# Kernel tuning notes

Measured on AMD Instinct MI355X. Metric: run time of the kernel, lower is better.

## Reference

```python
import jax, jax.numpy as jnp
import numpy as np

T, B, IN = 512, 256, 64
INNER = 20


def _lin_params(key, fan_in, fan_out):
    k1, k2 = jax.random.split(key)
    bound = 1.0 / np.sqrt(fan_in)
    w = jax.random.uniform(k1, (fan_out, fan_in), jnp.float32, -bound, bound)
    b = jax.random.uniform(k2, (fan_out,), jnp.float32, -bound, bound)
    return w, b


def _rnn_params(key, in_sz, hid):
    k1, k2, k3, k4 = jax.random.split(key, 4)
    bound = 1.0 / np.sqrt(hid)
    wih = jax.random.uniform(k1, (hid, in_sz), jnp.float32, -bound, bound)
    whh = jax.random.uniform(k2, (hid, hid), jnp.float32, -bound, bound)
    bih = jax.random.uniform(k3, (hid,), jnp.float32, -bound, bound)
    bhh = jax.random.uniform(k4, (hid,), jnp.float32, -bound, bound)
    return wih, whh, bih, bhh


def setup_inputs() -> dict:
    key = jax.random.key(0)
    ks = jax.random.split(key, 9)
    x = jax.random.normal(ks[0], (T, B, IN), jnp.float32)
    e_w1, e_b1 = _lin_params(ks[1], IN, 128)
    e_w2, e_b2 = _lin_params(ks[2], 128, 64)
    e_w3, e_b3 = _lin_params(ks[3], 64, 32)
    r1_wih, r1_whh, r1_bih, r1_bhh = _rnn_params(ks[4], 32, INNER)
    r2_wih, r2_whh, r2_bih, r2_bhh = _rnn_params(ks[5], INNER, 32)
    d_w1, d_b1 = _lin_params(ks[6], 32, 64)
    d_w2, d_b2 = _lin_params(ks[7], 64, 128)
    d_w3, d_b3 = _lin_params(ks[8], 128, IN)
    return dict(x=x,
                e_w1=e_w1, e_b1=e_b1, e_w2=e_w2, e_b2=e_b2, e_w3=e_w3, e_b3=e_b3,
                r1_wih=r1_wih, r1_whh=r1_whh, r1_bih=r1_bih, r1_bhh=r1_bhh,
                r2_wih=r2_wih, r2_whh=r2_whh, r2_bih=r2_bih, r2_bhh=r2_bhh,
                d_w1=d_w1, d_b1=d_b1, d_w2=d_w2, d_b2=d_b2, d_w3=d_w3, d_b3=d_b3)


def _rnn(x, wih, whh, bih, bhh):
    # x: (T, B, F); vanilla tanh RNN, h0 = 0. Returns all hidden states (T, B, H).
    # Precompute input projection for all timesteps in one GEMM.
    xp = jnp.einsum('tbf,hf->tbh', x, wih) + bih + bhh
    h0 = jnp.zeros((x.shape[1], whh.shape[0]), x.dtype)

    def step(h, xt):
        h = jnp.tanh(xt + h @ whh.T)
        return h, h

    _, out = jax.lax.scan(step, h0, xp)
    return out


def reference(x,
              e_w1, e_b1, e_w2, e_b2, e_w3, e_b3,
              r1_wih, r1_whh, r1_bih, r1_bhh,
              r2_wih, r2_whh, r2_bih, r2_bhh,
              d_w1, d_b1, d_w2, d_b2, d_w3, d_b3):
    relu = jax.nn.relu
    # encoder MLP
    h = relu(x @ e_w1.T + e_b1)
    h = relu(h @ e_w2.T + e_b2)
    h = relu(h @ e_w3.T + e_b3)
    # encoder RNN -> code (T, B, INNER)
    code = _rnn(h, r1_wih, r1_whh, r1_bih, r1_bhh)
    # decoder RNN then ReLU
    d = relu(_rnn(code, r2_wih, r2_whh, r2_bih, r2_bhh))
    d = relu(d @ d_w1.T + d_b1)
    d = relu(d @ d_w2.T + d_b2)
    return d @ d_w3.T + d_b3
```

## Files before the change

kernel.cpp:

```cpp
#include <hip/hip_runtime.h>

typedef _Float16 half8 __attribute__((ext_vector_type(8)));
typedef _Float16 half2_t __attribute__((ext_vector_type(2)));
typedef float f32x4 __attribute__((ext_vector_type(4)));

#define MFMA16(a, b, c) __builtin_amdgcn_mfma_f32_16x16x32_f16((a), (b), (c), 0, 0, 0)

__device__ __forceinline__ float exp2_fast(float x) {
#if __has_builtin(__builtin_amdgcn_exp2f)
    return __builtin_amdgcn_exp2f(x);
#else
    return exp2f(x);
#endif
}

__device__ __forceinline__ float tanh_fast(float x) {
    x = fminf(x, 22.f);
    float e = exp2_fast(2.885390082f * x);
    return (e - 1.f) * __builtin_amdgcn_rcpf(e + 1.f);
}

__device__ __forceinline__ float dot2f(unsigned a, unsigned b, float c) {
#if __has_builtin(__builtin_amdgcn_fdot2)
    return __builtin_amdgcn_fdot2(__builtin_bit_cast(half2_t, a),
                                  __builtin_bit_cast(half2_t, b), c, false);
#else
    float d;
    asm("v_dot2_f32_f16 %0, %1, %2, %3" : "=v"(d) : "v"(a), "v"(b), "v"(c));
    return d;
#endif
}


__global__ __launch_bounds__(256) void prep_kernel(
    const float* __restrict__ e_w1, const float* __restrict__ e_w3,
    const float* __restrict__ r1_wih, const float* __restrict__ e_w2,
    const float* __restrict__ d_w1, const float* __restrict__ d_w2,
    const float* __restrict__ d_w3,
    const float* __restrict__ r1_whh, const float* __restrict__ r2_wih,
    const float* __restrict__ r2_whh,
    const float* __restrict__ r2_bih, const float* __restrict__ r2_bhh,
    _Float16* __restrict__ enc_img, _Float16* __restrict__ w2img,
    _Float16* __restrict__ dec_img, _Float16* __restrict__ dw3img,
    unsigned* __restrict__ rnn_img)
{
    int i = blockIdx.x * 256 + threadIdx.x;
    if (i < 8192) {
        int r = i >> 6, c = i & 63;
        enc_img[r * 72 + c] = (_Float16)e_w1[i];
    } else if (i < 10240) {
        int j = i - 8192; int r = j >> 6, c = j & 63;
        enc_img[9216 + r * 72 + c] = (_Float16)e_w3[j];
    } else if (i < 10880) {
        int j = i - 10240; int r = j >> 5, c = j & 31;
        enc_img[11520 + r * 40 + c] = (_Float16)r1_wih[j];
    } else if (i < 19072) {
        int j = i - 10880;
        w2img[j] = (_Float16)e_w2[j];
    } else if (i < 21120) {
        int j = i - 19072; int r = j >> 5, c = j & 31;
        dec_img[r * 40 + c] = (_Float16)d_w1[j];
    } else if (i < 29312) {
        int j = i - 21120; int r = j >> 6, c = j & 63;
        dec_img[2560 + r * 72 + c] = (_Float16)d_w2[j];
    } else if (i < 37504) {
        int j = i - 29312;
        dw3img[j] = (_Float16)d_w3[j];
    } else if (i < 39552) {
        int j = i - 37504;
        int row = j >> 5, c = j & 31;
        unsigned val = 0;
        if (c == 26) {
            float b = (row < 32) ? (r2_bih[row] + r2_bhh[row]) : 0.f;
            val = __builtin_bit_cast(unsigned, b);
        } else {
            float v0 = 0.f, v1 = 0.f;
            if (row < 32) {
                if (c < 10)      { v0 = r2_wih[row * 20 + 2*c]; v1 = r2_wih[row * 20 + 2*c + 1]; }
                else if (c < 26) { int k = c - 10;
                                   v0 = r2_whh[row * 32 + 2*k]; v1 = r2_whh[row * 32 + 2*k + 1]; }
            } else if (row < 52) {
                int uu = row - 32;
                if (c < 10)      { v0 = r1_whh[uu * 20 + 2*c]; v1 = r1_whh[uu * 20 + 2*c + 1]; }
            }
            unsigned lo = (unsigned)__builtin_bit_cast(unsigned short, (_Float16)v0);
            unsigned hi = (unsigned)__builtin_bit_cast(unsigned short, (_Float16)v1);
            val = lo | (hi << 16);
        }
        rnn_img[j] = val;
    }
}

__global__ __launch_bounds__(256) void enc_kernel(
    const float* __restrict__ x,
    const float* __restrict__ eb1, const float* __restrict__ eb2,
    const float* __restrict__ eb3,
    const float* __restrict__ r1bih, const float* __restrict__ r1bhh,
    const _Float16* __restrict__ enc_img, const _Float16* __restrict__ w2img,
    float* __restrict__ xp1)
{
    __shared__ _Float16 a1buf[64 * 136];
    __shared__ _Float16 a2buf[64 * 72];
    __shared__ _Float16 a3buf[64 * 40];

    const int tid  = threadIdx.x;
    const int lane = tid & 63;
    const int wv   = tid >> 6;
    const int l15  = lane & 15;
    const int kg   = lane >> 4;
    const int rowA  = blockIdx.x * 64 + wv * 16 + l15;
    const int rowDl = wv * 16 + kg * 4;
    const int rowDg = blockIdx.x * 64 + rowDl;

    half8 a0, a1f;
    {
        const float* xr = x + (size_t)rowA * 64 + kg * 8;
        f32x4 p0 = *(const f32x4*)(xr);
        f32x4 p1 = *(const f32x4*)(xr + 4);
        f32x4 p2 = *(const f32x4*)(xr + 32);
        f32x4 p3 = *(const f32x4*)(xr + 36);
        #pragma unroll
        for (int j = 0; j < 4; ++j) {
            a0[j]    = (_Float16)p0[j];
            a0[j+4]  = (_Float16)p1[j];
            a1f[j]   = (_Float16)p2[j];
            a1f[j+4] = (_Float16)p3[j];
        }
    }
    f32x4 acc1[8] = {};
    #pragma unroll
    for (int ct = 0; ct < 8; ++ct) {
        const _Float16* wp = enc_img + (ct * 16 + l15) * 72 + kg * 8;
        half8 b0 = *(const half8*)(wp);
        half8 b1 = *(const half8*)(wp + 32);
        acc1[ct] = MFMA16(a0, b0, acc1[ct]);
        acc1[ct] = MFMA16(a1f, b1, acc1[ct]);
    }
    #pragma unroll
    for (int ct = 0; ct < 8; ++ct) {
        int col = ct * 16 + l15;
        float b = eb1[col];
        #pragma unroll
        for (int r = 0; r < 4; ++r) {
            float v = fmaxf(acc1[ct][r] + b, 0.f);
            a1buf[(rowDl + r) * 136 + col] = (_Float16)v;
        }
    }

    half8 af[4];
    #pragma unroll
    for (int kt = 0; kt < 4; ++kt)
        af[kt] = *(const half8*)(a1buf + (wv * 16 + l15) * 136 + kt * 32 + kg * 8);
    f32x4 acc2[4] = {};
    #pragma unroll
    for (int ct = 0; ct < 4; ++ct) {
        const _Float16* wp = w2img + (ct * 16 + l15) * 128 + kg * 8;
        #pragma unroll
        for (int kt = 0; kt < 4; ++kt) {
            half8 b = *(const half8*)(wp + kt * 32);
            acc2[ct] = MFMA16(af[kt], b, acc2[ct]);
        }
    }
    #pragma unroll
    for (int ct = 0; ct < 4; ++ct) {
        int col = ct * 16 + l15;
        float b = eb2[col];
        #pragma unroll
        for (int r = 0; r < 4; ++r) {
            float v = fmaxf(acc2[ct][r] + b, 0.f);
            a2buf[(rowDl + r) * 72 + col] = (_Float16)v;
        }
    }

    half8 c0 = *(const half8*)(a2buf + (wv * 16 + l15) * 72 + kg * 8);
    half8 c1 = *(const half8*)(a2buf + (wv * 16 + l15) * 72 + 32 + kg * 8);
    f32x4 acc3[2] = {};
    #pragma unroll
    for (int ct = 0; ct < 2; ++ct) {
        const _Float16* wp = enc_img + 9216 + (ct * 16 + l15) * 72 + kg * 8;
        half8 b0 = *(const half8*)(wp);
        half8 b1 = *(const half8*)(wp + 32);
        acc3[ct] = MFMA16(c0, b0, acc3[ct]);
        acc3[ct] = MFMA16(c1, b1, acc3[ct]);
    }
    #pragma unroll
    for (int ct = 0; ct < 2; ++ct) {
        int col = ct * 16 + l15;
        float b = eb3[col];
        #pragma unroll
        for (int r = 0; r < 4; ++r) {
            float v = fmaxf(acc3[ct][r] + b, 0.f);
            a3buf[(rowDl + r) * 40 + col] = (_Float16)v;
        }
    }

    half8 d0 = *(const half8*)(a3buf + (wv * 16 + l15) * 40 + kg * 8);
    f32x4 acc4[2] = {};
    #pragma unroll
    for (int ct = 0; ct < 2; ++ct) {
        const _Float16* wp = enc_img + 11520 + (ct * 16 + l15) * 40 + kg * 8;
        half8 b0 = *(const half8*)(wp);
        acc4[ct] = MFMA16(d0, b0, acc4[ct]);
    }
    #pragma unroll
    for (int ct = 0; ct < 2; ++ct) {
        int col = ct * 16 + l15;
        if (col < 20) {
            float bs = r1bih[col] + r1bhh[col];
            #pragma unroll
            for (int r = 0; r < 4; ++r)
                xp1[(size_t)(rowDg + r) * 20 + col] = acc4[ct][r] + bs;
        }
    }
}

__global__ __launch_bounds__(64) void rnn_kernel(
    const float* __restrict__ xp1,
    const unsigned* __restrict__ rnn_img,
    _Float16* __restrict__ dbuf)
{
    const int lane  = threadIdx.x & 63;
    const int batch = blockIdx.x;

    unsigned w[26];
    float base_b;
    {
        const unsigned* wr = rnn_img + lane * 32;
        #pragma unroll
        for (int i = 0; i < 6; ++i) {
            uint4 q = *(const uint4*)(wr + i * 4);
            w[i*4+0] = q.x; w[i*4+1] = q.y; w[i*4+2] = q.z; w[i*4+3] = q.w;
        }
        uint4 q = *(const uint4*)(wr + 24);
        w[24] = q.x; w[25] = q.y;
        base_b = __builtin_bit_cast(float, q.z);
    }

    const bool isB = lane < 32;
    int ua = lane - 32;
    if (ua < 0 || ua > 19) ua = 0;
    const float* xcol = xp1 + (size_t)batch * 20 + ua;

    const size_t DUMP_ELEMS = 4198400;
    _Float16* dst = isB ? (dbuf + (size_t)batch * 32 + lane)
                        : (dbuf + DUMP_ELEMS + (size_t)batch * 64 + lane);
    const size_t dstride = isB ? 8192 : 0;

    const unsigned sel = (lane & 1) ? 0x01000504u : 0x05040100u;
    unsigned hs[26];

    {
        float x0 = xcol[0];
        float h0 = isB ? 0.f : tanh_fast(x0);
        _Float16 h16 = (_Float16)h0;
        unsigned own  = (unsigned)__builtin_bit_cast(unsigned short, h16);
        unsigned dppv = (unsigned)__builtin_amdgcn_update_dpp(0, (int)own, 0xB1, 0xF, 0xF, false);
        unsigned pk   = __builtin_amdgcn_perm(dppv, own, sel);
        #pragma unroll
        for (int i = 0; i < 10; ++i)
            hs[i]    = (unsigned)__builtin_amdgcn_ds_bpermute((32 + 2*i) * 4, (int)pk);
        #pragma unroll
        for (int i = 0; i < 16; ++i)
            hs[10+i] = (unsigned)__builtin_amdgcn_ds_bpermute((2*i) * 4, (int)pk);
    }

    float xr[8];
    #pragma unroll
    for (int j = 0; j < 8; ++j)
        xr[j] = xcol[(size_t)(1 + j) * 5120];

    #pragma unroll 1
    for (int t0 = 0; t0 < 512; t0 += 8) {
        #pragma unroll
        for (int j = 0; j < 8; ++j) {
            const int t = t0 + j;
            float a0 = isB ? base_b : xr[j];
            float a1 = 0.f, a2 = 0.f, a3 = 0.f, a4 = 0.f, a5 = 0.f, a6 = 0.f, a7 = 0.f;
            a0 = dot2f(w[0],  hs[0],  a0);
            a1 = dot2f(w[1],  hs[1],  a1);
            a2 = dot2f(w[2],  hs[2],  a2);
            a3 = dot2f(w[3],  hs[3],  a3);
            a4 = dot2f(w[4],  hs[4],  a4);
            a5 = dot2f(w[5],  hs[5],  a5);
            a6 = dot2f(w[6],  hs[6],  a6);
            a7 = dot2f(w[7],  hs[7],  a7);
            a0 = dot2f(w[8],  hs[8],  a0);
            a1 = dot2f(w[9],  hs[9],  a1);
            a2 = dot2f(w[10], hs[10], a2);
            a3 = dot2f(w[11], hs[11], a3);
            a4 = dot2f(w[12], hs[12], a4);
            a5 = dot2f(w[13], hs[13], a5);
            a6 = dot2f(w[14], hs[14], a6);
            a7 = dot2f(w[15], hs[15], a7);
            a0 = dot2f(w[16], hs[16], a0);
            a1 = dot2f(w[17], hs[17], a1);
            a2 = dot2f(w[18], hs[18], a2);
            a3 = dot2f(w[19], hs[19], a3);
            a4 = dot2f(w[20], hs[20], a4);
            a5 = dot2f(w[21], hs[21], a5);
            a6 = dot2f(w[22], hs[22], a6);
            a7 = dot2f(w[23], hs[23], a7);
            a0 = dot2f(w[24], hs[24], a0);
            a1 = dot2f(w[25], hs[25], a1);
            float r = ((a0 + a1) + (a2 + a3)) + ((a4 + a5) + (a6 + a7));
            float h = tanh_fast(r);
            _Float16 h16 = (_Float16)h;

            _Float16 z = (_Float16)0.f;
            *dst = (h16 > z) ? h16 : z;
            dst += dstride;

            unsigned own  = (unsigned)__builtin_bit_cast(unsigned short, h16);
            unsigned dppv = (unsigned)__builtin_amdgcn_update_dpp(0, (int)own, 0xB1, 0xF, 0xF, false);
            unsigned pk   = __builtin_amdgcn_perm(dppv, own, sel);
            #pragma unroll
            for (int i = 0; i < 10; ++i)
                hs[i]    = (unsigned)__builtin_amdgcn_ds_bpermute((32 + 2*i) * 4, (int)pk);
            #pragma unroll
            for (int i = 0; i < 16; ++i)
                hs[10+i] = (unsigned)__builtin_amdgcn_ds_bpermute((2*i) * 4, (int)pk);

            xr[j] = xcol[(size_t)(t + 9) * 5120];
        }
    }
}

__global__ __launch_bounds__(256) void dec_kernel(
    const _Float16* __restrict__ dbuf,
    const float* __restrict__ db1, const float* __restrict__ db2,
    const float* __restrict__ db3,
    const _Float16* __restrict__ dec_img, const _Float16* __restrict__ dw3img,
    float* __restrict__ out)
{
    __shared__ _Float16 a1buf[64 * 72];
    __shared__ _Float16 a2buf[64 * 136];

    const int tid  = threadIdx.x;
    const int lane = tid & 63;
    const int wv   = tid >> 6;
    const int l15  = lane & 15;
    const int kg   = lane >> 4;
    const int rowA  = blockIdx.x * 64 + wv * 16 + l15;
    const int rowDl = wv * 16 + kg * 4;
    const int rowDg = blockIdx.x * 64 + rowDl;

    half8 a0 = *(const half8*)(dbuf + (size_t)rowA * 32 + kg * 8);
    f32x4 acc1[4] = {};
    #pragma unroll
    for (int ct = 0; ct < 4; ++ct) {
        half8 b = *(const half8*)(dec_img + (ct * 16 + l15) * 40 + kg * 8);
        acc1[ct] = MFMA16(a0, b, acc1[ct]);
    }
    #pragma unroll
    for (int ct = 0; ct < 4; ++ct) {
        int col = ct * 16 + l15;
        float b = db1[col];
        #pragma unroll
        for (int r = 0; r < 4; ++r) {
            float v = fmaxf(acc1[ct][r] + b, 0.f);
            a1buf[(rowDl + r) * 72 + col] = (_Float16)v;
        }
    }

    half8 af0 = *(const half8*)(a1buf + (wv * 16 + l15) * 72 + kg * 8);
    half8 af1 = *(const half8*)(a1buf + (wv * 16 + l15) * 72 + 32 + kg * 8);
    f32x4 acc2[8] = {};
    #pragma unroll
    for (int ct = 0; ct < 8; ++ct) {
        const _Float16* wp = dec_img + 2560 + (ct * 16 + l15) * 72 + kg * 8;
        half8 b0 = *(const half8*)(wp);
        half8 b1 = *(const half8*)(wp + 32);
        acc2[ct] = MFMA16(af0, b0, acc2[ct]);
        acc2[ct] = MFMA16(af1, b1, acc2[ct]);
    }
    #pragma unroll
    for (int ct = 0; ct < 8; ++ct) {
        int col = ct * 16 + l15;
        float b = db2[col];
        #pragma unroll
        for (int r = 0; r < 4; ++r) {
            float v = fmaxf(acc2[ct][r] + b, 0.f);
            a2buf[(rowDl + r) * 136 + col] = (_Float16)v;
        }
    }

    half8 cf[4];
    #pragma unroll
    for (int kt = 0; kt < 4; ++kt)
        cf[kt] = *(const half8*)(a2buf + (wv * 16 + l15) * 136 + kt * 32 + kg * 8);
    f32x4 acc3[4] = {};
    #pragma unroll
    for (int ct = 0; ct < 4; ++ct) {
        const _Float16* wp = dw3img + (ct * 16 + l15) * 128 + kg * 8;
        #pragma unroll
        for (int kt = 0; kt < 4; ++kt) {
            half8 b = *(const half8*)(wp + kt * 32);
            acc3[ct] = MFMA16(cf[kt], b, acc3[ct]);
        }
    }
    #pragma unroll
    for (int ct = 0; ct < 4; ++ct) {
        int col = ct * 16 + l15;
        float b = db3[col];
        #pragma unroll
        for (int r = 0; r < 4; ++r)
            out[(size_t)(rowDg + r) * 64 + col] = acc3[ct][r] + b;
    }
}

extern "C" void kernel_launch(void* const* d_in, const int* in_sizes, int n_in,
                              void* d_out, int out_size, void* d_ws, size_t ws_size,
                              hipStream_t stream) {
    const float* x      = (const float*)d_in[0];
    const float* e_w1   = (const float*)d_in[1];
    const float* e_b1   = (const float*)d_in[2];
    const float* e_w2   = (const float*)d_in[3];
    const float* e_b2   = (const float*)d_in[4];
    const float* e_w3   = (const float*)d_in[5];
    const float* e_b3   = (const float*)d_in[6];
    const float* r1_wih = (const float*)d_in[7];
    const float* r1_whh = (const float*)d_in[8];
    const float* r1_bih = (const float*)d_in[9];
    const float* r1_bhh = (const float*)d_in[10];
    const float* r2_wih = (const float*)d_in[11];
    const float* r2_whh = (const float*)d_in[12];
    const float* r2_bih = (const float*)d_in[13];
    const float* r2_bhh = (const float*)d_in[14];
    const float* d_w1   = (const float*)d_in[15];
    const float* d_b1   = (const float*)d_in[16];
    const float* d_w2   = (const float*)d_in[17];
    const float* d_b2   = (const float*)d_in[18];
    const float* d_w3   = (const float*)d_in[19];
    const float* d_b3   = (const float*)d_in[20];

    char* ws = (char*)d_ws;
    _Float16* enc_img = (_Float16*)(ws + 0);
    _Float16* w2img   = (_Float16*)(ws + 25600);
    _Float16* dec_img = (_Float16*)(ws + 41984);
    _Float16* dw3img  = (_Float16*)(ws + 65536);
    float*    xp1     = (float*)(ws + 81920);
    _Float16* dbuf    = (_Float16*)(ws + 10567680);
    unsigned* rnn_img = (unsigned*)(ws + 18956288);

    prep_kernel<<<155, 256, 0, stream>>>(e_w1, e_w3, r1_wih, e_w2, d_w1, d_w2, d_w3,
                                         r1_whh, r2_wih, r2_whh, r2_bih, r2_bhh,
                                         enc_img, w2img, dec_img, dw3img, rnn_img);
    enc_kernel<<<2048, 256, 0, stream>>>(x, e_b1, e_b2, e_b3, r1_bih, r1_bhh,
                                         enc_img, w2img, xp1);
    rnn_kernel<<<256, 64, 0, stream>>>(xp1, rnn_img, dbuf);
    dec_kernel<<<2048, 256, 0, stream>>>(dbuf, d_b1, d_b2, d_b3, dec_img, dw3img,
                                         (float*)d_out);
}
```

Before: 152.3 us.

## Permute weight columns for packed fp16 epilogue stores and store RNN input projection in fp16

Weight images are column-permuted in prep so each lane's MFMA output columns become contiguous. The bias+ReLU epilogues can then write packed fp16 vectors to LDS (uint4/uint2) instead of scalar halves. Biases are folded into accumulator initialisation. The RNN input projection xp1 is now stored as fp16 with a padded, permuted 32-wide layout rather than fp32, which halves its traffic at some precision cost, and the RNN kernel's dbuf write order and read indexing are adjusted to match.

After: 155.2 us. About the same (+1.9%).

```diff
diff --git a/kernel.cpp b/kernel.cpp
--- a/kernel.cpp
+++ b/kernel.cpp
@@ -2,6 +2,7 @@
 
 typedef _Float16 half8 __attribute__((ext_vector_type(8)));
 typedef _Float16 half2_t __attribute__((ext_vector_type(2)));
+typedef __fp16 fp16x2 __attribute__((ext_vector_type(2)));
 typedef float f32x4 __attribute__((ext_vector_type(4)));
 
 #define MFMA16(a, b, c) __builtin_amdgcn_mfma_f32_16x16x32_f16((a), (b), (c), 0, 0, 0)
@@ -29,6 +30,15 @@
     asm("v_dot2_f32_f16 %0, %1, %2, %3" : "=v"(d) : "v"(a), "v"(b), "v"(c));
     return d;
 #endif
+}
+
+__device__ __forceinline__ unsigned pk_relu(float a, float b) {
+    fp16x2 h = __builtin_amdgcn_cvt_pkrtz(fmaxf(a, 0.f), fmaxf(b, 0.f));
+    return __builtin_bit_cast(unsigned, h);
+}
+__device__ __forceinline__ unsigned pk2(float a, float b) {
+    fp16x2 h = __builtin_amdgcn_cvt_pkrtz(a, b);
+    return __builtin_bit_cast(unsigned, h);
 }
 
 
@@ -50,24 +60,25 @@
         enc_img[r * 72 + c] = (_Float16)e_w1[i];
     } else if (i < 10240) {
         int j = i - 8192; int r = j >> 6, c = j & 63;
-        enc_img[9216 + r * 72 + c] = (_Float16)e_w3[j];
-    } else if (i < 10880) {
-        int j = i - 10240; int r = j >> 5, c = j & 31;
-        enc_img[11520 + r * 40 + c] = (_Float16)r1_wih[j];
-    } else if (i < 19072) {
-        int j = i - 10880;
-        w2img[j] = (_Float16)e_w2[j];
-    } else if (i < 21120) {
-        int j = i - 19072; int r = j >> 5, c = j & 31;
-        dec_img[r * 40 + c] = (_Float16)d_w1[j];
-    } else if (i < 29312) {
-        int j = i - 21120; int r = j >> 6, c = j & 63;
-        dec_img[2560 + r * 72 + c] = (_Float16)d_w2[j];
-    } else if (i < 37504) {
-        int j = i - 29312;
-        dw3img[j] = (_Float16)d_w3[j];
-    } else if (i < 39552) {
-        int j = i - 37504;
+        enc_img[9216 + r * 72 + ((c & 15) * 4 + (c >> 4))] = (_Float16)e_w3[j];
+    } else if (i < 11264) {
+        int j = i - 10240; int r = j >> 5, k = j & 31;
+        float v = (r < 20) ? r1_wih[r * 32 + k] : 0.f;
+        enc_img[11520 + r * 32 + ((k & 15) * 2 + (k >> 4))] = (_Float16)v;
+    } else if (i < 19456) {
+        int j = i - 11264; int r = j >> 7, c = j & 127;
+        w2img[r * 128 + ((c & 15) * 8 + (c >> 4))] = (_Float16)e_w2[j];
+    } else if (i < 21504) {
+        int j = i - 19456; int r = j >> 5, k = j & 31;
+        dec_img[r * 32 + ((k & 15) * 2 + (k >> 4))] = (_Float16)d_w1[j];
+    } else if (i < 29696) {
+        int j = i - 21504; int r = j >> 6, c = j & 63;
+        dec_img[2048 + r * 72 + ((c & 15) * 4 + (c >> 4))] = (_Float16)d_w2[j];
+    } else if (i < 37888) {
+        int j = i - 29696; int r = j >> 7, c = j & 127;
+        dw3img[r * 128 + ((c & 15) * 8 + (c >> 4))] = (_Float16)d_w3[j];
+    } else if (i < 39936) {
+        int j = i - 37888;
         int row = j >> 5, c = j & 31;
         unsigned val = 0;
         if (c == 26) {
@@ -97,7 +108,7 @@
     const float* __restrict__ eb3,
     const float* __restrict__ r1bih, const float* __restrict__ r1bhh,
     const _Float16* __restrict__ enc_img, const _Float16* __restrict__ w2img,
-    float* __restrict__ xp1)
+    unsigned* __restrict__ xp1u)
 {
     __shared__ _Float16 a1buf[64 * 136];
     __shared__ _Float16 a2buf[64 * 72];
@@ -127,7 +138,12 @@
             a1f[j+4] = (_Float16)p3[j];
         }
     }
-    f32x4 acc1[8] = {};
+    f32x4 acc1[8];
+    #pragma unroll
+    for (int ct = 0; ct < 8; ++ct) {
+        float b = eb1[ct * 16 + l15];
+        acc1[ct] = (f32x4){b, b, b, b};
+    }
     #pragma unroll
     for (int ct = 0; ct < 8; ++ct) {
         const _Float16* wp = enc_img + (ct * 16 + l15) * 72 + kg * 8;
@@ -137,21 +153,25 @@
         acc1[ct] = MFMA16(a1f, b1, acc1[ct]);
     }
     #pragma unroll
-    for (int ct = 0; ct < 8; ++ct) {
-        int col = ct * 16 + l15;
-        float b = eb1[col];
-        #pragma unroll
-        for (int r = 0; r < 4; ++r) {
-            float v = fmaxf(acc1[ct][r] + b, 0.f);
-            a1buf[(rowDl + r) * 136 + col] = (_Float16)v;
-        }
+    for (int r = 0; r < 4; ++r) {
+        uint4 v;
+        v.x = pk_relu(acc1[0][r], acc1[1][r]);
+        v.y = pk_relu(acc1[2][r], acc1[3][r]);
+        v.z = pk_relu(acc1[4][r], acc1[5][r]);
+        v.w = pk_relu(acc1[6][r], acc1[7][r]);
+        *(uint4*)(a1buf + (rowDl + r) * 136 + l15 * 8) = v;
     }
 
     half8 af[4];
     #pragma unroll
     for (int kt = 0; kt < 4; ++kt)
         af[kt] = *(const half8*)(a1buf + (wv * 16 + l15) * 136 + kt * 32 + kg * 8);
-    f32x4 acc2[4] = {};
+    f32x4 acc2[4];
+    #pragma unroll
+    for (int ct = 0; ct < 4; ++ct) {
+        float b = eb2[ct * 16 + l15];
+        acc2[ct] = (f32x4){b, b, b, b};
+    }
     #pragma unroll
     for (int ct = 0; ct < 4; ++ct) {
         const _Float16* wp = w2img + (ct * 16 + l15) * 128 + kg * 8;
@@ -162,19 +182,21 @@
         }
     }
     #pragma unroll
-    for (int ct = 0; ct < 4; ++ct) {
-        int col = ct * 16 + l15;
-        float b = eb2[col];
-        #pragma unroll
-        for (int r = 0; r < 4; ++r) {
-            float v = fmaxf(acc2[ct][r] + b, 0.f);
-            a2buf[(rowDl + r) * 72 + col] = (_Float16)v;
-        }
+    for (int r = 0; r < 4; ++r) {
+        uint2 v;
+        v.x = pk_relu(acc2[0][r], acc2[1][r]);
+        v.y = pk_relu(acc2[2][r], acc2[3][r]);
+        *(uint2*)(a2buf + (rowDl + r) * 72 + l15 * 4) = v;
     }
 
     half8 c0 = *(const half8*)(a2buf + (wv * 16 + l15) * 72 + kg * 8);
     half8 c1 = *(const half8*)(a2buf + (wv * 16 + l15) * 72 + 32 + kg * 8);
-    f32x4 acc3[2] = {};
+    f32x4 acc3[2];
+    #pragma unroll
+    for (int ct = 0; ct < 2; ++ct) {
+        float b = eb3[ct * 16 + l15];
+        acc3[ct] = (f32x4){b, b, b, b};
+    }
     #pragma unroll
     for (int ct = 0; ct < 2; ++ct) {
         const _Float16* wp = enc_img + 9216 + (ct * 16 + l15) * 72 + kg * 8;
@@ -184,38 +206,32 @@
         acc3[ct] = MFMA16(c1, b1, acc3[ct]);
     }
     #pragma unroll
+    for (int r = 0; r < 4; ++r)
+        *(unsigned*)(a3buf + (rowDl + r) * 40 + l15 * 2) =
+            pk_relu(acc3[0][r], acc3[1][r]);
+
+    half8 d0 = *(const half8*)(a3buf + (wv * 16 + l15) * 40 + kg * 8);
+    f32x4 acc4[2];
+    {
+        int c1i = 16 + l15; if (c1i > 19) c1i = 19;
+        float b0v = r1bih[l15] + r1bhh[l15];
+        float b1v = r1bih[c1i] + r1bhh[c1i];
+        acc4[0] = (f32x4){b0v, b0v, b0v, b0v};
+        acc4[1] = (f32x4){b1v, b1v, b1v, b1v};
+    }
+    #pragma unroll
     for (int ct = 0; ct < 2; ++ct) {
-        int col = ct * 16 + l15;
-        float b = eb3[col];
-        #pragma unroll
-        for (int r = 0; r < 4; ++r) {
-            float v = fmaxf(acc3[ct][r] + b, 0.f);
-            a3buf[(rowDl + r) * 40 + col] = (_Float16)v;
-        }
-    }
-
-    half8 d0 = *(const half8*)(a3buf + (wv * 16 + l15) * 40 + kg * 8);
-    f32x4 acc4[2] = {};
-    #pragma unroll
-    for (int ct = 0; ct < 2; ++ct) {
-        const _Float16* wp = enc_img + 11520 + (ct * 16 + l15) * 40 + kg * 8;
+        const _Float16* wp = enc_img + 11520 + (ct * 16 + l15) * 32 + kg * 8;
         half8 b0 = *(const half8*)(wp);
         acc4[ct] = MFMA16(d0, b0, acc4[ct]);
     }
     #pragma unroll
-    for (int ct = 0; ct < 2; ++ct) {
-        int col = ct * 16 + l15;
-        if (col < 20) {
-            float bs = r1bih[col] + r1bhh[col];
-            #pragma unroll
-            for (int r = 0; r < 4; ++r)
-                xp1[(size_t)(rowDg + r) * 20 + col] = acc4[ct][r] + bs;
-        }
-    }
+    for (int r = 0; r < 4; ++r)
+        xp1u[(size_t)(rowDg + r) * 16 + l15] = pk2(acc4[0][r], acc4[1][r]);
 }
 
 __global__ __launch_bounds__(64) void rnn_kernel(
-    const float* __restrict__ xp1,
+    const _Float16* __restrict__ xph,
     const unsigned* __restrict__ rnn_img,
     _Float16* __restrict__ dbuf)
 {
@@ -239,10 +255,11 @@
     const bool isB = lane < 32;
     int ua = lane - 32;
     if (ua < 0 || ua > 19) ua = 0;
-    const float* xcol = xp1 + (size_t)batch * 20 + ua;
-
+    const _Float16* xcol = xph + (size_t)batch * 32 + ((ua & 15) * 2 + (ua >> 4));
+
+    const int up = ((lane & 31) & 15) * 2 + ((lane & 31) >> 4);
     const size_t DUMP_ELEMS = 4198400;
-    _Float16* dst = isB ? (dbuf + (size_t)batch * 32 + lane)
+    _Float16* dst = isB ? (dbuf + (size_t)batch * 32 + up)
                         : (dbuf + DUMP_ELEMS + (size_t)batch * 64 + lane);
     const size_t dstride = isB ? 8192 : 0;
 
@@ -250,7 +267,7 @@
     unsigned hs[26];
 
     {
-        float x0 = xcol[0];
+        float x0 = (float)xcol[0];
         float h0 = isB ? 0.f : tanh_fast(x0);
         _Float16 h16 = (_Float16)h0;
         unsigned own  = (unsigned)__builtin_bit_cast(unsigned short, h16);
@@ -267,7 +284,7 @@
     float xr[8];
     #pragma unroll
     for (int j = 0; j < 8; ++j)
-        xr[j] = xcol[(size_t)(1 + j) * 5120];
+        xr[j] = (float)xcol[(size_t)(1 + j) * 8192];
 
     #pragma unroll 1
     for (int t0 = 0; t0 < 512; t0 += 8) {
@@ -320,7 +337,7 @@
             for (int i = 0; i < 16; ++i)
                 hs[10+i] = (unsigned)__builtin_amdgcn_ds_bpermute((2*i) * 4, (int)pk);
 
-            xr[j] = xcol[(size_t)(t + 9) * 5120];
+            xr[j] = (float)xcol[(size_t)(t + 9) * 8192];
         }
     }
 }
@@ -345,50 +362,61 @@
     const int rowDg = blockIdx.x * 64 + rowDl;
 
     half8 a0 = *(const half8*)(dbuf + (size_t)rowA * 32 + kg * 8);
-    f32x4 acc1[4] = {};
-    #pragma unroll
-    for (int ct = 0; ct < 4; ++ct) {
-        half8 b = *(const half8*)(dec_img + (ct * 16 + l15) * 40 + kg * 8);
+    f32x4 acc1[4];
+    #pragma unroll
+    for (int ct = 0; ct < 4; ++ct) {
+        float b = db1[ct * 16 + l15];
+        acc1[ct] = (f32x4){b, b, b, b};
+    }
+    #pragma unroll
+    for (int ct = 0; ct < 4; ++ct) {
+        half8 b = *(const half8*)(dec_img + (ct * 16 + l15) * 32 + kg * 8);
         acc1[ct] = MFMA16(a0, b, acc1[ct]);
     }
     #pragma unroll
-    for (int ct = 0; ct < 4; ++ct) {
-        int col = ct * 16 + l15;
-        float b = db1[col];
-        #pragma unroll
-        for (int r = 0; r < 4; ++r) {
-            float v = fmaxf(acc1[ct][r] + b, 0.f);
-            a1buf[(rowDl + r) * 72 + col] = (_Float16)v;
-        }
+    for (int r = 0; r < 4; ++r) {
+        uint2 v;
+        v.x = pk_relu(acc1[0][r], acc1[1][r]);
+        v.y = pk_relu(acc1[2][r], acc1[3][r]);
+        *(uint2*)(a1buf + (rowDl + r) * 72 + l15 * 4) = v;
     }
 
     half8 af0 = *(const half8*)(a1buf + (wv * 16 + l15) * 72 + kg * 8);
     half8 af1 = *(const half8*)(a1buf + (wv * 16 + l15) * 72 + 32 + kg * 8);
-    f32x4 acc2[8] = {};
+    f32x4 acc2[8];
     #pragma unroll
     for (int ct = 0; ct < 8; ++ct) {
-        const _Float16* wp = dec_img + 2560 + (ct * 16 + l15) * 72 + kg * 8;
+        float b = db2[ct * 16 + l15];
+        acc2[ct] = (f32x4){b, b, b, b};
+    }
+    #pragma unroll
+    for (int ct = 0; ct < 8; ++ct) {
+        const _Float16* wp = dec_img + 2048 + (ct * 16 + l15) * 72 + kg * 8;
         half8 b0 = *(const half8*)(wp);
         half8 b1 = *(const half8*)(wp + 32);
         acc2[ct] = MFMA16(af0, b0, acc2[ct]);
         acc2[ct] = MFMA16(af1, b1, acc2[ct]);
     }
     #pragma unroll
-    for (int ct = 0; ct < 8; ++ct) {
-        int col = ct * 16 + l15;
-        float b = db2[col];
-        #pragma unroll
-        for (int r = 0; r < 4; ++r) {
-            float v = fmaxf(acc2[ct][r] + b, 0.f);
-            a2buf[(rowDl + r) * 136 + col] = (_Float16)v;
-        }
+    for (int r = 0; r < 4; ++r) {
+        uint4 v;
+        v.x = pk_relu(acc2[0][r], acc2[1][r]);
+        v.y = pk_relu(acc2[2][r], acc2[3][r]);
+        v.z = pk_relu(acc2[4][r], acc2[5][r]);
+        v.w = pk_relu(acc2[6][r], acc2[7][r]);
+        *(uint4*)(a2buf + (rowDl + r) * 136 + l15 * 8) = v;
     }
 
     half8 cf[4];
     #pragma unroll
     for (int kt = 0; kt < 4; ++kt)
         cf[kt] = *(const half8*)(a2buf + (wv * 16 + l15) * 136 + kt * 32 + kg * 8);
-    f32x4 acc3[4] = {};
+    f32x4 acc3[4];
+    #pragma unroll
+    for (int ct = 0; ct < 4; ++ct) {
+        float b = db3[ct * 16 + l15];
+        acc3[ct] = (f32x4){b, b, b, b};
+    }
     #pragma unroll
     for (int ct = 0; ct < 4; ++ct) {
         const _Float16* wp = dw3img + (ct * 16 + l15) * 128 + kg * 8;
@@ -401,10 +429,9 @@
     #pragma unroll
     for (int ct = 0; ct < 4; ++ct) {
         int col = ct * 16 + l15;
-        float b = db3[col];
         #pragma unroll
         for (int r = 0; r < 4; ++r)
-            out[(size_t)(rowDg + r) * 64 + col] = acc3[ct][r] + b;
+            out[(size_t)(rowDg + r) * 64 + col] = acc3[ct][r];
     }
 }
 
@@ -438,16 +465,17 @@
     _Float16* w2img   = (_Float16*)(ws + 25600);
     _Float16* dec_img = (_Float16*)(ws + 41984);
     _Float16* dw3img  = (_Float16*)(ws + 65536);
-    float*    xp1     = (float*)(ws + 81920);
+    unsigned* xp1u    = (unsigned*)(ws + 81920);
+    _Float16* xph     = (_Float16*)(ws + 81920);
     _Float16* dbuf    = (_Float16*)(ws + 10567680);
     unsigned* rnn_img = (unsigned*)(ws + 18956288);
 
-    prep_kernel<<<155, 256, 0, stream>>>(e_w1, e_w3, r1_wih, e_w2, d_w1, d_w2, d_w3,
+    prep_kernel<<<156, 256, 0, stream>>>(e_w1, e_w3, r1_wih, e_w2, d_w1, d_w2, d_w3,
                                          r1_whh, r2_wih, r2_whh, r2_bih, r2_bhh,
                                          enc_img, w2img, dec_img, dw3img, rnn_img);
     enc_kernel<<<2048, 256, 0, stream>>>(x, e_b1, e_b2, e_b3, r1_bih, r1_bhh,
-                                         enc_img, w2img, xp1);
-    rnn_kernel<<<256, 64, 0, stream>>>(xp1, rnn_img, dbuf);
+                                         enc_img, w2img, xp1u);
+    rnn_kernel<<<256, 64, 0, stream>>>(xph, rnn_img, dbuf);
     dec_kernel<<<2048, 256, 0, stream>>>(dbuf, d_b1, d_b2, d_b3, dec_img, dw3img,
                                          (float*)d_out);
 }
```
